# Performance work log

Hardware: AMD Instinct MI355X
Metric: run time of the kernel (lower is better)

## Reference

```python
import jax, jax.numpy as jnp
import numpy as np

T, N = 32, 256
HID, NL = 64, 1
D_CH, Hg, Wg = 2, 8, 8            # obs shape (2, 8, 8); d must be 2 to match Conv2d(2*HID, 2*HID)
NSUB, SUBDIM = 6, 3               # subtasks shape (n_subtasks, subtask_dim)
OBS_V, SUB_V, NACT = 16, 20, 6    # vocab sizes; action_space.n = NSUB
OBS_LEN = D_CH * Hg * Wg          # 128
SUB_LEN = NSUB * SUBDIM           # 18
GRU_IN = HID * (OBS_LEN + SUBDIM) # 8384
STATE = 2 + NL * HID + NACT + NSUB  # a(1)+v(1)+h(64)+a_probs(6)+p(6) = 78


def setup_inputs() -> dict:
    key = jax.random.key(0)
    ks = jax.random.split(key, 12)
    obs_idx = jax.random.randint(ks[0], (T, N, OBS_LEN), 0, OBS_V)
    sub_idx = jax.random.randint(ks[1], (T, N, SUB_LEN), 0, SUB_V)
    act = jax.random.randint(ks[2], (T, N, 1), 0, NACT)  # all >= 0 -> sample_new is a no-op
    inputs = jnp.concatenate([obs_idx, sub_idx, act], -1).astype(jnp.float32)
    hx = jnp.zeros((1, N, STATE), jnp.float32)  # all-zero -> new_episode everywhere
    sd = lambda f: 1.0 / np.sqrt(f)
    return dict(
        inputs=inputs,
        hx=hx,
        subtask_emb=jax.random.normal(ks[3], (SUB_V, HID)),
        obs_emb=jax.random.normal(ks[4], (OBS_V, HID)),
        conv_w=jax.random.normal(ks[5], (2 * HID, 2 * HID)) * sd(2 * HID),
        conv_b=jnp.zeros((2 * HID,)),
        w_ih=jax.random.normal(ks[6], (3 * HID, GRU_IN)) * sd(GRU_IN),
        w_hh=jax.random.normal(ks[7], (3 * HID, HID)) * sd(HID),
        b_ih=jnp.zeros((3 * HID,)),
        b_hh=jnp.zeros((3 * HID,)),
        critic_w=jax.random.normal(ks[8], (1, HID)) * sd(HID),
        critic_b=jnp.zeros((1,)),
        phi_w=jax.random.normal(ks[9], (1, HID)) * sd(HID),
        phi_b=jnp.zeros((1,)),
    )


def _forward(inputs, hx, subtask_emb, obs_emb, conv_w, conv_b, w_ih, w_hh,
             b_ih, b_hh, critic_w, critic_b, phi_w, phi_b):
    ints = inputs.astype(jnp.int32)
    obs_all = ints[:, :, :OBS_LEN]                      # (T,N,128)
    sub_all = ints[:, :, OBS_LEN:OBS_LEN + SUB_LEN]     # (T,N,18)
    act_all = ints[:, :, -1]                            # (T,N)

    # subtask memory from first timestep: (N, NSUB, SUBDIM*HID)
    M = subtask_emb[sub_all[0]].reshape(N, NSUB, SUBDIM * HID)

    hx0 = hx[0]
    new_episode = jnp.all(hx0 == 0, axis=-1)            # (N,)
    # recurrent state split order a(1), v(1), h(NL*HID), a_probs(NACT), p(NSUB)
    h0 = hx0[:, 2:2 + NL * HID].reshape(N, NL, HID).transpose(1, 0, 2)  # (NL,N,HID)
    p0 = hx0[:, 2 + NL * HID + NACT:]
    p0 = p0.at[:, 0].set(jnp.where(new_episode, 1.0, p0[:, 0]))

    def gru_cell(x, h):
        gx = x @ w_ih.T + b_ih
        gh = h @ w_hh.T + b_hh
        r = jax.nn.sigmoid(gx[:, :HID] + gh[:, :HID])
        z = jax.nn.sigmoid(gx[:, HID:2 * HID] + gh[:, HID:2 * HID])
        n = jnp.tanh(gx[:, 2 * HID:] + r * gh[:, 2 * HID:])
        return (1 - z) * n + z * h

    def step(carry, xt):
        h, p = carry
        obs_t, act_t = xt
        r_vec = jnp.einsum('ns,nsk->nk', p, M)          # (p.unsqueeze(1) @ M).squeeze(1)
        emb = obs_emb[obs_t.reshape(N, D_CH, Hg, Wg)]   # (N,2,H,W,HID)
        conv_in = emb.transpose(0, 1, 4, 2, 3).reshape(N, 2 * HID, Hg * Wg)
        conv_out = jnp.einsum('ncp,oc->nop', conv_in, conv_w) + conv_b[None, :, None]  # 1x1 conv
        gru_in = jnp.concatenate([conv_out.reshape(N, -1), r_vec], -1)
        hn = gru_cell(gru_in, h[0])                     # single-layer GRU, seq len 1
        h_new = hn[None]
        c = jax.nn.sigmoid(hn @ phi_w.T + phi_b)        # (N,1)
        # torch.roll(F.pad(p,(0,1)), 1) flattened: pad column is 0, so this is a
        # right-shift with 0 fill; p1[:, -1] == p[:, -1].
        p1 = jnp.concatenate([jnp.zeros((N, 1), p.dtype), p[:, :-1]], axis=1)
        p2 = p1 + p * p[:, -1:]
        p_new = (1 - c) * p + c * p2
        probs = p_new / p_new.sum(-1, keepdims=True)    # FixedCategorical(p).probs
        v = hn @ critic_w.T + critic_b                  # (N,1)
        a = act_t.astype(jnp.float32)[:, None]          # actions all >=0 -> no resampling
        h_flat = h_new.transpose(1, 0, 2).reshape(N, -1)
        ys = jnp.concatenate([a, v, h_flat, probs, p_new], -1)
        return (h_new, p_new), ys

    _, hx_out = jax.lax.scan(step, (h0, p0), (obs_all, act_all))  # (T,N,78)
    return hx_out


def reference(inputs, hx, subtask_emb, obs_emb, conv_w, conv_b, w_ih, w_hh,
              b_ih, b_hh, critic_w, critic_b, phi_w, phi_b):
    hx_out = _forward(inputs, hx, subtask_emb, obs_emb, conv_w, conv_b, w_ih,
                      w_hh, b_ih, b_hh, critic_w, critic_b, phi_w, phi_b)
    return (hx_out, hx_out[-1:])
```

## Files before the change

### kernel.cpp

```cpp
#include <hip/hip_runtime.h>
#include <hip/hip_bf16.h>
#include <math.h>

#define TT 32
#define NN 256
#define HID 64
#define OBS_LEN 128
#define SUB_LEN 18
#define IN_ROW 147
#define GJ 192
#define GRU_IN 8384
#define STATE 78
#define NSUB 6
#define NT_TILES 1572

typedef __fp16 half2_t __attribute__((ext_vector_type(2)));

__device__ __forceinline__ float sigm(float x) {
    return 1.0f / (1.0f + __expf(-x));
}

__device__ __forceinline__ unsigned short f2bf(float f) {
    unsigned u = __float_as_uint(f);
    u += 0x7fffu + ((u >> 16) & 1u);
    return (unsigned short)(u >> 16);
}

#if defined(__has_builtin)
#if __has_builtin(__builtin_amdgcn_fdot2)
#define HAVE_FDOT2 1
#endif
#endif

__device__ __forceinline__ float fdot2(half2_t a, half2_t b, float c) {
#ifdef HAVE_FDOT2
    return __builtin_amdgcn_fdot2(a, b, c, false);
#else
    return fmaf((float)a.x, (float)b.x, fmaf((float)a.y, (float)b.y, c));
#endif
}

__global__ __launch_bounds__(256) void k_TGC(const float* __restrict__ w_ih,
                                             const float* __restrict__ obs_emb,
                                             const float* __restrict__ conv_w,
                                             const float* __restrict__ conv_b,
                                             const float* __restrict__ b_ih,
                                             float* __restrict__ wT,
                                             float* __restrict__ G,
                                             float* __restrict__ CB2) {
    int b = blockIdx.x;
    int tid = threadIdx.x;
    __shared__ float tile[32][33];
    __shared__ float red[4];

    if (b < NT_TILES) {
        int bx = b % 262, by = b / 262;
        int i0 = bx * 32, j0 = by * 32;
        int tx = tid & 31, ty = tid >> 5;
        #pragma unroll
        for (int a = 0; a < 4; a++)
            tile[ty + a * 8][tx] = w_ih[(size_t)(j0 + ty + a * 8) * GRU_IN + i0 + tx];
        __syncthreads();
        #pragma unroll
        for (int a = 0; a < 4; a++)
            wT[(size_t)(i0 + ty + a * 8) * GJ + j0 + tx] = tile[tx][ty + a * 8];
    } else if (b < NT_TILES + 16) {
        int i = (b - NT_TILES) * 256 + tid;
        int v = i & 15, d = (i >> 4) & 1, o = i >> 5;
        float acc = 0.f;
        const float* oe = obs_emb + v * 64;
        const float* cw = conv_w + o * 128 + d * 64;
        #pragma unroll
        for (int hd = 0; hd < 64; hd++) acc = fmaf(oe[hd], cw[hd], acc);
        G[i] = acc;
    } else {
        int j = b - (NT_TILES + 16);
        const float* wr = w_ih + (size_t)j * GRU_IN;
        float acc = 0.f;
        #pragma unroll 8
        for (int i = tid; i < 8192; i += 256) acc = fmaf(conv_b[i >> 6], wr[i], acc);
        for (int off = 32; off > 0; off >>= 1) acc += __shfl_down(acc, off, 64);
        if ((tid & 63) == 0) red[tid >> 6] = acc;
        __syncthreads();
        if (tid == 0) CB2[j] = b_ih[j] + red[0] + red[1] + red[2] + red[3];
    }
}

__global__ __launch_bounds__(192, 4) void k_EQ(const float* __restrict__ inputs,
                                               const float* __restrict__ subtask_emb,
                                               const float* __restrict__ G,
                                               const float* __restrict__ wT,
                                               unsigned short* __restrict__ E16,
                                               float* __restrict__ Q) {
    int b = blockIdx.x;
    int j = threadIdx.x;

    if (b < 256) {
        int dp = b >> 1, half = b & 1;
        int d = dp >> 6, p = dp & 63;
        __shared__ __align__(16) float Gs[128 * 8];
        for (int e = j; e < 1024; e += GJ) {
            int o = e >> 3, vv = e & 7;
            Gs[e] = G[(o << 5) + (d << 4) + (half << 3) + vv];
        }
        __syncthreads();
        float acc[8];
        #pragma unroll
        for (int v = 0; v < 8; v++) acc[v] = 0.f;
        const float* wb = wT + (size_t)p * GJ + j;
        #pragma unroll 16
        for (int o = 0; o < 128; o++) {
            float w = wb[(size_t)(o * 64) * GJ];
            float4 g0 = *(const float4*)&Gs[o * 8];
            float4 g1 = *(const float4*)&Gs[o * 8 + 4];
            acc[0] = fmaf(g0.x, w, acc[0]);
            acc[1] = fmaf(g0.y, w, acc[1]);
            acc[2] = fmaf(g0.z, w, acc[2]);
            acc[3] = fmaf(g0.w, w, acc[3]);
            acc[4] = fmaf(g1.x, w, acc[4]);
            acc[5] = fmaf(g1.y, w, acc[5]);
            acc[6] = fmaf(g1.z, w, acc[6]);
            acc[7] = fmaf(g1.w, w, acc[7]);
        }
        unsigned short* Eo = E16 + ((size_t)(dp * 16 + half * 8)) * GJ;
        #pragma unroll
        for (int v = 0; v < 8; v++) Eo[v * GJ + j] = f2bf(acc[v]);
    } else {
        int n = b - 256;
        __shared__ int sidx[SUB_LEN];
        __shared__ __align__(16) float Ms[GJ * 8];
        if (j < SUB_LEN) sidx[j] = (int)inputs[(size_t)n * IN_ROW + OBS_LEN + j];
        __syncthreads();
        for (int e = j; e < NSUB * GJ; e += GJ) {
            int s = e / GJ, k = e - s * GJ;
            int row = sidx[s * 3 + (k >> 6)];
            Ms[k * 8 + s] = subtask_emb[row * 64 + (k & 63)];
        }
        __syncthreads();
        float acc[NSUB] = {0.f, 0.f, 0.f, 0.f, 0.f, 0.f};
        const float* base = wT + (size_t)8192 * GJ + j;
        #pragma unroll 8
        for (int k = 0; k < GJ; k++) {
            float w = base[(size_t)k * GJ];
            float4 m0 = *(const float4*)&Ms[k * 8];
            float2 m1 = *(const float2*)&Ms[k * 8 + 4];
            acc[0] = fmaf(m0.x, w, acc[0]);
            acc[1] = fmaf(m0.y, w, acc[1]);
            acc[2] = fmaf(m0.z, w, acc[2]);
            acc[3] = fmaf(m0.w, w, acc[3]);
            acc[4] = fmaf(m1.x, w, acc[4]);
            acc[5] = fmaf(m1.y, w, acc[5]);
        }
        for (int s = 0; s < NSUB; s++) Q[((size_t)n * NSUB + s) * GJ + j] = acc[s];
    }
}

__global__ __launch_bounds__(192, 4) void k_gx(const float* __restrict__ inputs,
                                               const unsigned short* __restrict__ E16,
                                               const float* __restrict__ CB2,
                                               float* __restrict__ gx_all) {
    int tn0 = blockIdx.x * 4;
    int tid = threadIdx.x;
    __shared__ __align__(16) int off[4][OBS_LEN];
    for (int e = tid; e < 4 * OBS_LEN; e += 192) {
        int row = e >> 7, dp = e & 127;
        int id = (int)inputs[(size_t)(tn0 + row) * IN_ROW + dp];
        off[row][dp] = (dp * 16 + id) * 384;
    }
    __syncthreads();
    int r = tid / 48, l = tid - r * 48;
    int jj = l * 4;
    int tn = tn0 + r;
    const char* base = (const char*)E16 + jj * 2;
    float4 cb = *(const float4*)(CB2 + jj);
    float a0 = cb.x, a1 = cb.y, a2 = cb.z, a3 = cb.w;
    const int* id = off[r];
    #pragma unroll
    for (int dq = 0; dq < 8; dq++) {
        int4 o0 = *(const int4*)&id[dq * 16];
        int4 o1 = *(const int4*)&id[dq * 16 + 4];
        int4 o2 = *(const int4*)&id[dq * 16 + 8];
        int4 o3 = *(const int4*)&id[dq * 16 + 12];
        uint2 u0 = *(const uint2*)(base + o0.x);
        uint2 u1 = *(const uint2*)(base + o0.y);
        uint2 u2 = *(const uint2*)(base + o0.z);
        uint2 u3 = *(const uint2*)(base + o0.w);
        uint2 u4 = *(const uint2*)(base + o1.x);
        uint2 u5 = *(const uint2*)(base + o1.y);
        uint2 u6 = *(const uint2*)(base + o1.z);
        uint2 u7 = *(const uint2*)(base + o1.w);
        uint2 u8 = *(const uint2*)(base + o2.x);
        uint2 u9 = *(const uint2*)(base + o2.y);
        uint2 uA = *(const uint2*)(base + o2.z);
        uint2 uB = *(const uint2*)(base + o2.w);
        uint2 uC = *(const uint2*)(base + o3.x);
        uint2 uD = *(const uint2*)(base + o3.y);
        uint2 uE = *(const uint2*)(base + o3.z);
        uint2 uF = *(const uint2*)(base + o3.w);
        #define ACC(u) do { \
            a0 += __uint_as_float((u).x << 16); \
            a1 += __uint_as_float((u).x & 0xffff0000u); \
            a2 += __uint_as_float((u).y << 16); \
            a3 += __uint_as_float((u).y & 0xffff0000u); } while (0)
        ACC(u0); ACC(u1); ACC(u2); ACC(u3);
        ACC(u4); ACC(u5); ACC(u6); ACC(u7);
        ACC(u8); ACC(u9); ACC(uA); ACC(uB);
        ACC(uC); ACC(uD); ACC(uE); ACC(uF);
        #undef ACC
    }
    float4 o4; o4.x = a0; o4.y = a1; o4.z = a2; o4.w = a3;
    *(float4*)(gx_all + (size_t)tn * GJ + jj) = o4;
}

__global__ __launch_bounds__(64, 1) void k_rec(const float* __restrict__ inputs,
                                               const float* __restrict__ hx,
                                               const float* __restrict__ w_hh,
                                               const float* __restrict__ b_hh,
                                               const float* __restrict__ critic_w,
                                               const float* __restrict__ critic_b,
                                               const float* __restrict__ phi_w,
                                               const float* __restrict__ phi_b,
                                               const float* __restrict__ Q,
                                               const float* __restrict__ gx_all,
                                               float* __restrict__ out) {
    int n = blockIdx.x;
    int lane = threadIdx.x;

    __shared__ __align__(16) float gx_lds[TT * GJ];
    __shared__ __align__(16) __fp16 h16[64];
    __shared__ float h_all[TT][65];
    __shared__ float cw_sh[64];
    __shared__ float act_sh[TT];

    for (int e = lane * 4; e < TT * GJ; e += 64 * 4) {
        int t = e / GJ, j = e - t * GJ;
        *(float4*)&gx_lds[e] = *(const float4*)(gx_all + ((size_t)t * NN + n) * GJ + j);
    }
    if (lane < TT)
        act_sh[lane] = inputs[((size_t)lane * NN + n) * IN_ROW + (IN_ROW - 1)];

    half2_t wv0[32], wv1[32], wv2[32];
    {
        const float4* r0 = (const float4*)(w_hh + (size_t)lane * 64);
        const float4* r1 = (const float4*)(w_hh + (size_t)(64 + lane) * 64);
        const float4* r2 = (const float4*)(w_hh + (size_t)(128 + lane) * 64);
        #pragma unroll
        for (int h4 = 0; h4 < 16; h4++) {
            float4 a = r0[h4];
            wv0[2*h4]   = __builtin_amdgcn_cvt_pkrtz(a.x, a.y);
            wv0[2*h4+1] = __builtin_amdgcn_cvt_pkrtz(a.z, a.w);
            float4 c = r1[h4];
            wv1[2*h4]   = __builtin_amdgcn_cvt_pkrtz(c.x, c.y);
            wv1[2*h4+1] = __builtin_amdgcn_cvt_pkrtz(c.z, c.w);
            float4 d = r2[h4];
            wv2[2*h4]   = __builtin_amdgcn_cvt_pkrtz(d.x, d.y);
            wv2[2*h4+1] = __builtin_amdgcn_cvt_pkrtz(d.z, d.w);
        }
    }
    half2_t ph[32];
    {
        const float4* pp = (const float4*)phi_w;
        #pragma unroll
        for (int h4 = 0; h4 < 16; h4++) {
            float4 a = pp[h4];
            ph[2*h4]   = __builtin_amdgcn_cvt_pkrtz(a.x, a.y);
            ph[2*h4+1] = __builtin_amdgcn_cvt_pkrtz(a.z, a.w);
        }
    }
    float q0[NSUB], q1[NSUB], q2[NSUB];
    #pragma unroll
    for (int s = 0; s < NSUB; s++) {
        const float* qb = Q + ((size_t)n * NSUB + s) * GJ;
        q0[s] = qb[lane]; q1[s] = qb[64 + lane]; q2[s] = qb[128 + lane];
    }
    float bh0 = b_hh[lane], bh1 = b_hh[64 + lane], bh2 = b_hh[128 + lane];
    cw_sh[lane] = critic_w[lane];
    float phib = phi_b[0], crtb = critic_b[0];

    float v0 = hx[(size_t)n * STATE + lane];
    float v1 = (lane < STATE - 64) ? hx[(size_t)n * STATE + 64 + lane] : 0.f;
    unsigned long long bal0 = __ballot(v0 != 0.f);
    unsigned long long bal1 = __ballot((lane < STATE - 64) && v1 != 0.f);
    bool ne = ((bal0 | bal1) == 0ULL);
    float h_own = hx[(size_t)n * STATE + 2 + lane];
    float p0, p1, p2, p3, p4, p5;
    {
        const float* pb = hx + (size_t)n * STATE + 72;
        p0 = pb[0]; p1 = pb[1]; p2 = pb[2]; p3 = pb[3]; p4 = pb[4]; p5 = pb[5];
    }
    if (ne) p0 = 1.0f;
    h16[lane] = (__fp16)h_own;

    auto finalize = [&](int tf, float pc) {
        float c = sigm(pc + phib);
        float n0 = fmaf(c, (p0 * p5)      - p0, p0);
        float n1 = fmaf(c, (p0 + p1 * p5) - p1, p1);
        float n2 = fmaf(c, (p1 + p2 * p5) - p2, p2);
        float n3 = fmaf(c, (p2 + p3 * p5) - p3, p3);
        float n4 = fmaf(c, (p3 + p4 * p5) - p4, p4);
        float n5 = fmaf(c, (p4 + p5 * p5) - p5, p5);
        float psum = ((n0 + n1) + (n2 + n3)) + (n4 + n5);
        float rinv = 1.0f / psum;
        if (lane < 12) {
            int s = (lane < 6) ? lane : lane - 6;
            float pp = n0;
            pp = (s == 1) ? n1 : pp;
            pp = (s == 2) ? n2 : pp;
            pp = (s == 3) ? n3 : pp;
            pp = (s == 4) ? n4 : pp;
            pp = (s == 5) ? n5 : pp;
            size_t fb = ((size_t)tf * NN + n) * STATE;
            out[fb + ((lane < 6) ? (72 + lane) : (66 + lane - 6))] =
                (lane < 6) ? pp : pp * rinv;
        }
        p0 = n0; p1 = n1; p2 = n2; p3 = n3; p4 = n4; p5 = n5;
    };

    for (int t = 0; t < TT; t++) {
        uint4 raw[8];
        #pragma unroll
        for (int rix = 0; rix < 8; rix++) raw[rix] = ((const uint4*)h16)[rix];
        half2_t h2[32];
        {
            const unsigned* rw = (const unsigned*)raw;
            #pragma unroll
            for (int k = 0; k < 32; k++) h2[k] = __builtin_bit_cast(half2_t, rw[k]);
        }

        float A0 = 0.f, B0 = 0.f, C0 = 0.f, D0 = 0.f;
        float A1 = 0.f, B1 = 0.f, C1 = 0.f, D1 = 0.f;
        float A2 = 0.f, B2 = 0.f, C2 = 0.f, D2 = 0.f;
        float PA = 0.f, PB = 0.f, PC = 0.f, PD = 0.f;
        #pragma unroll
        for (int k = 0; k < 8; k++) {
            A0 = fdot2(h2[k], wv0[k], A0);
            B0 = fdot2(h2[8 + k], wv0[8 + k], B0);
            C0 = fdot2(h2[16 + k], wv0[16 + k], C0);
            D0 = fdot2(h2[24 + k], wv0[24 + k], D0);
            A1 = fdot2(h2[k], wv1[k], A1);
            B1 = fdot2(h2[8 + k], wv1[8 + k], B1);
            C1 = fdot2(h2[16 + k], wv1[16 + k], C1);
            D1 = fdot2(h2[24 + k], wv1[24 + k], D1);
            A2 = fdot2(h2[k], wv2[k], A2);
            B2 = fdot2(h2[8 + k], wv2[8 + k], B2);
            C2 = fdot2(h2[16 + k], wv2[16 + k], C2);
            D2 = fdot2(h2[24 + k], wv2[24 + k], D2);
            PA = fdot2(h2[k], ph[k], PA);
            PB = fdot2(h2[8 + k], ph[8 + k], PB);
            PC = fdot2(h2[16 + k], ph[16 + k], PC);
            PD = fdot2(h2[24 + k], ph[24 + k], PD);
        }
        float pc = (PA + PB) + (PC + PD);

        if (t > 0) finalize(t - 1, pc);

        float gx0 = gx_lds[t * GJ + lane];
        float gx1 = gx_lds[t * GJ + 64 + lane];
        float gx2 = gx_lds[t * GJ + 128 + lane];
        gx0 = fmaf(p0, q0[0], gx0); gx1 = fmaf(p0, q1[0], gx1); gx2 = fmaf(p0, q2[0], gx2);
        gx0 = fmaf(p1, q0[1], gx0); gx1 = fmaf(p1, q1[1], gx1); gx2 = fmaf(p1, q2[1], gx2);
        gx0 = fmaf(p2, q0[2], gx0); gx1 = fmaf(p2, q1[2], gx1); gx2 = fmaf(p2, q2[2], gx2);
        gx0 = fmaf(p3, q0[3], gx0); gx1 = fmaf(p3, q1[3], gx1); gx2 = fmaf(p3, q2[3], gx2);
        gx0 = fmaf(p4, q0[4], gx0); gx1 = fmaf(p4, q1[4], gx1); gx2 = fmaf(p4, q2[4], gx2);
        gx0 = fmaf(p5, q0[5], gx0); gx1 = fmaf(p5, q1[5], gx1); gx2 = fmaf(p5, q2[5], gx2);

        float gh0 = bh0 + (A0 + B0) + (C0 + D0);
        float gh1 = bh1 + (A1 + B1) + (C1 + D1);
        float gh2 = bh2 + (A2 + B2) + (C2 + D2);

        float r = sigm(gx0 + gh0);
        float z = sigm(gx1 + gh1);
        float x2 = fmaf(r, gh2, gx2);
        float e2 = __expf(2.f * x2);
        float nv = 1.f - 2.f / (e2 + 1.f);
        float hn = fmaf(z, h_own - nv, nv);

        h16[lane] = (__fp16)hn;
        h_all[t][lane] = hn;

        size_t base = ((size_t)t * NN + n) * STATE;
        out[base + 2 + lane] = hn;
        if (lane == 1) out[base + 0] = act_sh[t];

        h_own = hn;
    }

    {
        uint4 raw[8];
        #pragma unroll
        for (int rix = 0; rix < 8; rix++) raw[rix] = ((const uint4*)h16)[rix];
        const unsigned* rw = (const unsigned*)raw;
        float PA = 0.f, PB = 0.f;
        #pragma unroll
        for (int k = 0; k < 16; k++) {
            PA = fdot2(__builtin_bit_cast(half2_t, rw[k]), ph[k], PA);
            PB = fdot2(__builtin_bit_cast(half2_t, rw[16 + k]), ph[16 + k], PB);
        }
        finalize(TT - 1, PA + PB);
    }

    float vlast;
    {
        int tp = lane >> 1, half = lane & 1;
        const float* hr = &h_all[tp][half * 32];
        const float* cr = &cw_sh[half * 32];
        float vc = 0.f;
        #pragma unroll
        for (int k = 0; k < 32; k++) vc = fmaf(hr[k], cr[k], vc);
        vc += __shfl_xor(vc, 1, 64);
        float vt = vc + crtb;
        if (half == 0) out[((size_t)tp * NN + n) * STATE + 1] = vt;
        vlast = __shfl(vt, 62, 64);
    }

    {
        float psum = ((p0 + p1) + (p2 + p3)) + (p4 + p5);
        float rinv = 1.0f / psum;
        size_t fs = (size_t)TT * NN * STATE + (size_t)n * STATE;
        out[fs + 2 + lane] = h_own;
        if (lane < 12) {
            int s = (lane < 6) ? lane : lane - 6;
            float pp = p0;
            pp = (s == 1) ? p1 : pp;
            pp = (s == 2) ? p2 : pp;
            pp = (s == 3) ? p3 : pp;
            pp = (s == 4) ? p4 : pp;
            pp = (s == 5) ? p5 : pp;
            out[fs + ((lane < 6) ? (72 + lane) : (66 + lane - 6))] =
                (lane < 6) ? pp : pp * rinv;
        } else if (lane == 12) {
            out[fs + 0] = act_sh[TT - 1];
        } else if (lane == 13) {
            out[fs + 1] = vlast;
        }
    }
}

extern "C" void kernel_launch(void* const* d_in, const int* in_sizes, int n_in,
                              void* d_out, int out_size, void* d_ws, size_t ws_size,
                              hipStream_t stream) {
    const float* inputs      = (const float*)d_in[0];
    const float* hx          = (const float*)d_in[1];
    const float* subtask_emb = (const float*)d_in[2];
    const float* obs_emb     = (const float*)d_in[3];
    const float* conv_w      = (const float*)d_in[4];
    const float* conv_b      = (const float*)d_in[5];
    const float* w_ih        = (const float*)d_in[6];
    const float* w_hh        = (const float*)d_in[7];
    const float* b_ih        = (const float*)d_in[8];
    const float* b_hh        = (const float*)d_in[9];
    const float* critic_w    = (const float*)d_in[10];
    const float* critic_b    = (const float*)d_in[11];
    const float* phi_w       = (const float*)d_in[12];
    const float* phi_b       = (const float*)d_in[13];
    float* out = (float*)d_out;

    float* ws   = (float*)d_ws;
    float* wT   = ws;
    float* G    = wT + (size_t)GRU_IN * GJ;
    float* CB2  = G + 4096;
    float* Ef   = CB2 + 192;
    unsigned short* E16 = (unsigned short*)Ef;
    float* Q    = Ef + 196608;
    float* gx   = Q + (size_t)NN * NSUB * GJ;

    k_TGC<<<NT_TILES + 16 + GJ, 256, 0, stream>>>(w_ih, obs_emb, conv_w, conv_b,
                                                  b_ih, wT, G, CB2);
    k_EQ<<<512, GJ, 0, stream>>>(inputs, subtask_emb, G, wT, E16, Q);
    k_gx<<<TT * NN / 4, GJ, 0, stream>>>(inputs, E16, CB2, gx);
    k_rec<<<NN, 64, 0, stream>>>(inputs, hx, w_hh, b_hh, critic_w, critic_b,
                                 phi_w, phi_b, Q, gx, out);
}
```

Before: 163.8 us.

## Drop w_ih transpose kernel and fuse G/CB2 computation into the E/Q kernel

Removes the separate kernel that transposed w_ih into a workspace and precomputed G and CB2. The E/Q kernel now reads w_ih directly in its native row layout, recomputes G per block from conv_w and obs_emb staged in LDS, and gains extra blocks that compute the conv-bias projection CB2. Because CB2 is now produced in the same launch that k_gx would otherwise wait on, the bias add moves from k_gx into k_rec's gx load. This saves one launch and the full transpose write/read, at the cost of strided per-thread w_ih reads and redundant G computation in every block.

```diff
diff --git a/kernel.cpp b/kernel.cpp
--- a/kernel.cpp
+++ b/kernel.cpp
@@ -12,7 +12,6 @@
 #define GRU_IN 8384
 #define STATE 78
 #define NSUB 6
-#define NT_TILES 1572
 
 typedef __fp16 half2_t __attribute__((ext_vector_type(2)));
 
@@ -40,77 +39,55 @@
 #endif
 }
 
-__global__ __launch_bounds__(256) void k_TGC(const float* __restrict__ w_ih,
-                                             const float* __restrict__ obs_emb,
-                                             const float* __restrict__ conv_w,
-                                             const float* __restrict__ conv_b,
-                                             const float* __restrict__ b_ih,
-                                             float* __restrict__ wT,
-                                             float* __restrict__ G,
-                                             float* __restrict__ CB2) {
-    int b = blockIdx.x;
-    int tid = threadIdx.x;
-    __shared__ float tile[32][33];
-    __shared__ float red[4];
-
-    if (b < NT_TILES) {
-        int bx = b % 262, by = b / 262;
-        int i0 = bx * 32, j0 = by * 32;
-        int tx = tid & 31, ty = tid >> 5;
-        #pragma unroll
-        for (int a = 0; a < 4; a++)
-            tile[ty + a * 8][tx] = w_ih[(size_t)(j0 + ty + a * 8) * GRU_IN + i0 + tx];
-        __syncthreads();
-        #pragma unroll
-        for (int a = 0; a < 4; a++)
-            wT[(size_t)(i0 + ty + a * 8) * GJ + j0 + tx] = tile[tx][ty + a * 8];
-    } else if (b < NT_TILES + 16) {
-        int i = (b - NT_TILES) * 256 + tid;
-        int v = i & 15, d = (i >> 4) & 1, o = i >> 5;
-        float acc = 0.f;
-        const float* oe = obs_emb + v * 64;
-        const float* cw = conv_w + o * 128 + d * 64;
-        #pragma unroll
-        for (int hd = 0; hd < 64; hd++) acc = fmaf(oe[hd], cw[hd], acc);
-        G[i] = acc;
-    } else {
-        int j = b - (NT_TILES + 16);
-        const float* wr = w_ih + (size_t)j * GRU_IN;
-        float acc = 0.f;
-        #pragma unroll 8
-        for (int i = tid; i < 8192; i += 256) acc = fmaf(conv_b[i >> 6], wr[i], acc);
-        for (int off = 32; off > 0; off >>= 1) acc += __shfl_down(acc, off, 64);
-        if ((tid & 63) == 0) red[tid >> 6] = acc;
-        __syncthreads();
-        if (tid == 0) CB2[j] = b_ih[j] + red[0] + red[1] + red[2] + red[3];
-    }
-}
-
-__global__ __launch_bounds__(192, 4) void k_EQ(const float* __restrict__ inputs,
-                                               const float* __restrict__ subtask_emb,
-                                               const float* __restrict__ G,
-                                               const float* __restrict__ wT,
-                                               unsigned short* __restrict__ E16,
-                                               float* __restrict__ Q) {
+__global__ __launch_bounds__(192, 4) void k_EQC(const float* __restrict__ inputs,
+                                                const float* __restrict__ subtask_emb,
+                                                const float* __restrict__ obs_emb,
+                                                const float* __restrict__ conv_w,
+                                                const float* __restrict__ conv_b,
+                                                const float* __restrict__ w_ih,
+                                                const float* __restrict__ b_ih,
+                                                unsigned short* __restrict__ E16,
+                                                float* __restrict__ Q,
+                                                float* __restrict__ CB2) {
     int b = blockIdx.x;
     int j = threadIdx.x;
+
+    __shared__ __align__(16) float cw_sh[128 * 65];
+    __shared__ __align__(16) float obs_sh[8 * 65];
+    __shared__ __align__(16) float Gs[128 * 8];
+    __shared__ __align__(16) float Ms[GJ * 8];
+    __shared__ int sidx[SUB_LEN];
+    __shared__ float red[3];
 
     if (b < 256) {
         int dp = b >> 1, half = b & 1;
         int d = dp >> 6, p = dp & 63;
-        __shared__ __align__(16) float Gs[128 * 8];
+        for (int e = j; e < 8192; e += GJ) {
+            int o = e >> 6, hd = e & 63;
+            cw_sh[o * 65 + hd] = conv_w[o * 128 + d * 64 + hd];
+        }
+        for (int e = j; e < 512; e += GJ) {
+            int vv = e >> 6, hd = e & 63;
+            obs_sh[vv * 65 + hd] = obs_emb[(half * 8 + vv) * 64 + hd];
+        }
+        __syncthreads();
         for (int e = j; e < 1024; e += GJ) {
             int o = e >> 3, vv = e & 7;
-            Gs[e] = G[(o << 5) + (d << 4) + (half << 3) + vv];
+            const float* oe = &obs_sh[vv * 65];
+            const float* cw = &cw_sh[o * 65];
+            float acc = 0.f;
+            #pragma unroll
+            for (int hd = 0; hd < 64; hd++) acc = fmaf(oe[hd], cw[hd], acc);
+            Gs[e] = acc;
         }
         __syncthreads();
         float acc[8];
         #pragma unroll
         for (int v = 0; v < 8; v++) acc[v] = 0.f;
-        const float* wb = wT + (size_t)p * GJ + j;
+        const float* wrow = w_ih + (size_t)j * GRU_IN + p;
         #pragma unroll 16
         for (int o = 0; o < 128; o++) {
-            float w = wb[(size_t)(o * 64) * GJ];
+            float w = wrow[o * 64];
             float4 g0 = *(const float4*)&Gs[o * 8];
             float4 g1 = *(const float4*)&Gs[o * 8 + 4];
             acc[0] = fmaf(g0.x, w, acc[0]);
@@ -125,10 +102,8 @@
         unsigned short* Eo = E16 + ((size_t)(dp * 16 + half * 8)) * GJ;
         #pragma unroll
         for (int v = 0; v < 8; v++) Eo[v * GJ + j] = f2bf(acc[v]);
-    } else {
+    } else if (b < 512) {
         int n = b - 256;
-        __shared__ int sidx[SUB_LEN];
-        __shared__ __align__(16) float Ms[GJ * 8];
         if (j < SUB_LEN) sidx[j] = (int)inputs[(size_t)n * IN_ROW + OBS_LEN + j];
         __syncthreads();
         for (int e = j; e < NSUB * GJ; e += GJ) {
@@ -138,26 +113,40 @@
         }
         __syncthreads();
         float acc[NSUB] = {0.f, 0.f, 0.f, 0.f, 0.f, 0.f};
-        const float* base = wT + (size_t)8192 * GJ + j;
+        const float* wrow = w_ih + (size_t)j * GRU_IN + 8192;
         #pragma unroll 8
-        for (int k = 0; k < GJ; k++) {
-            float w = base[(size_t)k * GJ];
-            float4 m0 = *(const float4*)&Ms[k * 8];
-            float2 m1 = *(const float2*)&Ms[k * 8 + 4];
-            acc[0] = fmaf(m0.x, w, acc[0]);
-            acc[1] = fmaf(m0.y, w, acc[1]);
-            acc[2] = fmaf(m0.z, w, acc[2]);
-            acc[3] = fmaf(m0.w, w, acc[3]);
-            acc[4] = fmaf(m1.x, w, acc[4]);
-            acc[5] = fmaf(m1.y, w, acc[5]);
+        for (int k = 0; k < GJ; k += 4) {
+            float4 w4 = *(const float4*)&wrow[k];
+            #pragma unroll
+            for (int kk = 0; kk < 4; kk++) {
+                float w = (kk == 0) ? w4.x : (kk == 1) ? w4.y : (kk == 2) ? w4.z : w4.w;
+                float4 m0 = *(const float4*)&Ms[(k + kk) * 8];
+                float2 m1 = *(const float2*)&Ms[(k + kk) * 8 + 4];
+                acc[0] = fmaf(m0.x, w, acc[0]);
+                acc[1] = fmaf(m0.y, w, acc[1]);
+                acc[2] = fmaf(m0.z, w, acc[2]);
+                acc[3] = fmaf(m0.w, w, acc[3]);
+                acc[4] = fmaf(m1.x, w, acc[4]);
+                acc[5] = fmaf(m1.y, w, acc[5]);
+            }
         }
         for (int s = 0; s < NSUB; s++) Q[((size_t)n * NSUB + s) * GJ + j] = acc[s];
+    } else {
+        int jr = b - 512;
+        const float* wr = w_ih + (size_t)jr * GRU_IN;
+        float acc = 0.f;
+        #pragma unroll 8
+        for (int i = j; i < 8192; i += GJ) acc = fmaf(conv_b[i >> 6], wr[i], acc);
+        #pragma unroll
+        for (int off = 32; off > 0; off >>= 1) acc += __shfl_down(acc, off, 64);
+        if ((j & 63) == 0) red[j >> 6] = acc;
+        __syncthreads();
+        if (j == 0) CB2[jr] = b_ih[jr] + red[0] + red[1] + red[2];
     }
 }
 
 __global__ __launch_bounds__(192, 4) void k_gx(const float* __restrict__ inputs,
                                                const unsigned short* __restrict__ E16,
-                                               const float* __restrict__ CB2,
                                                float* __restrict__ gx_all) {
     int tn0 = blockIdx.x * 4;
     int tid = threadIdx.x;
@@ -172,8 +161,7 @@
     int jj = l * 4;
     int tn = tn0 + r;
     const char* base = (const char*)E16 + jj * 2;
-    float4 cb = *(const float4*)(CB2 + jj);
-    float a0 = cb.x, a1 = cb.y, a2 = cb.z, a3 = cb.w;
+    float a0 = 0.f, a1 = 0.f, a2 = 0.f, a3 = 0.f;
     const int* id = off[r];
     #pragma unroll
     for (int dq = 0; dq < 8; dq++) {
@@ -222,6 +210,7 @@
                                                const float* __restrict__ phi_b,
                                                const float* __restrict__ Q,
                                                const float* __restrict__ gx_all,
+                                               const float* __restrict__ CB2,
                                                float* __restrict__ out) {
     int n = blockIdx.x;
     int lane = threadIdx.x;
@@ -234,7 +223,10 @@
 
     for (int e = lane * 4; e < TT * GJ; e += 64 * 4) {
         int t = e / GJ, j = e - t * GJ;
-        *(float4*)&gx_lds[e] = *(const float4*)(gx_all + ((size_t)t * NN + n) * GJ + j);
+        float4 v = *(const float4*)(gx_all + ((size_t)t * NN + n) * GJ + j);
+        float4 c = *(const float4*)(CB2 + j);
+        v.x += c.x; v.y += c.y; v.z += c.z; v.w += c.w;
+        *(float4*)&gx_lds[e] = v;
     }
     if (lane < TT)
         act_sh[lane] = inputs[((size_t)lane * NN + n) * IN_ROW + (IN_ROW - 1)];
@@ -456,18 +448,15 @@
     float* out = (float*)d_out;
 
     float* ws   = (float*)d_ws;
-    float* wT   = ws;
-    float* G    = wT + (size_t)GRU_IN * GJ;
-    float* CB2  = G + 4096;
+    float* CB2  = ws;
     float* Ef   = CB2 + 192;
     unsigned short* E16 = (unsigned short*)Ef;
     float* Q    = Ef + 196608;
     float* gx   = Q + (size_t)NN * NSUB * GJ;
 
-    k_TGC<<<NT_TILES + 16 + GJ, 256, 0, stream>>>(w_ih, obs_emb, conv_w, conv_b,
-                                                  b_ih, wT, G, CB2);
-    k_EQ<<<512, GJ, 0, stream>>>(inputs, subtask_emb, G, wT, E16, Q);
-    k_gx<<<TT * NN / 4, GJ, 0, stream>>>(inputs, E16, CB2, gx);
+    k_EQC<<<704, GJ, 0, stream>>>(inputs, subtask_emb, obs_emb, conv_w, conv_b,
+                                  w_ih, b_ih, E16, Q, CB2);
+    k_gx<<<TT * NN / 4, GJ, 0, stream>>>(inputs, E16, gx);
     k_rec<<<NN, 64, 0, stream>>>(inputs, hx, w_hh, b_hh, critic_w, critic_b,
-                                 phi_w, phi_b, Q, gx, out);
-}
+                                 phi_w, phi_b, Q, gx, CB2, out);
+}
```

Result: slower. 174.7 us (+6.6%).
